# Performance work log

Measured on AMD Instinct MI355X. Metric: run time of the kernel, lower is better.

The kernel has to match this reference:

```python
import jax, jax.numpy as jnp
import numpy as np

COST_POS = 5.0
COST_CONF = 1.0
LAMBDA_POS = 5.0
LAMBDA_CONF = 2.0
LAMBDA_NOOBJ = 0.5


def _lsa(cost):
    """Rectangular linear sum assignment (Jonker-Volgenant shortest augmenting
    path), same semantics as scipy.optimize.linear_sum_assignment."""
    cost = np.asarray(cost, dtype=np.float64)
    transposed = cost.shape[1] < cost.shape[0]
    if transposed:
        cost = cost.T
    nr, nc = cost.shape  # nr <= nc
    u = np.zeros(nr)
    v = np.zeros(nc)
    col4row = np.full(nr, -1, dtype=np.int64)
    row4col = np.full(nc, -1, dtype=np.int64)
    for cur_row in range(nr):
        shortest = np.full(nc, np.inf)
        pathback = np.full(nc, -1, dtype=np.int64)
        SR = np.zeros(nr, dtype=bool)
        SC = np.zeros(nc, dtype=bool)
        remaining = np.ones(nc, dtype=bool)
        min_val = 0.0
        i = cur_row
        sink = -1
        while sink == -1:
            SR[i] = True
            rem = np.flatnonzero(remaining)
            new_cost = min_val + cost[i, rem] - u[i] - v[rem]
            better = new_cost < shortest[rem]
            idx = rem[better]
            shortest[idx] = new_cost[better]
            pathback[idx] = i
            j = rem[np.argmin(shortest[rem])]
            min_val = shortest[j]
            remaining[j] = False
            SC[j] = True
            if row4col[j] == -1:
                sink = j
            else:
                i = row4col[j]
        u[cur_row] += min_val
        rows = np.flatnonzero(SR)
        rows = rows[rows != cur_row]
        u[rows] += min_val - shortest[col4row[rows]]
        v[SC] -= min_val - shortest[SC]
        j = sink
        while True:
            i = pathback[j]
            row4col[j] = i
            col4row[i], j = j, col4row[i]
            if i == cur_row:
                break
    if transposed:
        rows = col4row
        cols = np.arange(nr)
        order = np.argsort(rows)
        return rows[order], cols[order]
    return np.arange(nr), col4row


def _match(pred_c, conf, gt_c):
    """Per-image Hungarian matching (host-side, @no_grad in the original).
    cost = COST_POS * L1(pred, gt) - COST_CONF * sigmoid(conf)."""
    B, N, _ = pred_c.shape
    M = gt_c.shape[1]
    pred_idx = np.empty((B, M), dtype=np.int64)
    gt_idx = np.empty((B, M), dtype=np.int64)
    for b in range(B):
        c_pos = np.abs(pred_c[b][:, None, :] - gt_c[b][None, :, :]).sum(-1)  # [N,M]
        c_conf = -1.0 / (1.0 + np.exp(-conf[b]))  # [N]
        cost = COST_POS * c_pos + COST_CONF * c_conf[:, None]
        r, c = _lsa(cost)
        pred_idx[b] = r
        gt_idx[b] = c
    return pred_idx, gt_idx


def setup_inputs() -> dict:
    key = jax.random.key(0)
    B, N, M, D = 32, 300, 50, 2
    k1, k2, k3, k4, k5 = jax.random.split(key, 5)
    return {
        "pred_centroids": jax.random.uniform(k1, (B, N, D), dtype=jnp.float32),
        "pred_logits": jax.random.normal(k2, (B, N, 1), dtype=jnp.float32),
        "pred_conf": jax.random.normal(k3, (B, N), dtype=jnp.float32),
        "gt_centroids": jax.random.uniform(k4, (B, M, D), dtype=jnp.float32),
        "gt_classes": jax.random.randint(k5, (B, M), 0, 1),
    }


def reference(pred_centroids, pred_logits, pred_conf, gt_centroids, gt_classes):
    B, N, D = pred_centroids.shape
    M = gt_centroids.shape[1]
    # Matching indices are constants (computed under no_grad, host-side).
    pred_idx, gt_idx = _match(np.asarray(pred_centroids, np.float64),
                              np.asarray(pred_conf, np.float64),
                              np.asarray(gt_centroids, np.float64))
    pred_idx = jnp.asarray(pred_idx)  # [B,M]
    gt_idx = jnp.asarray(gt_idx)      # [B,M]
    b = jnp.arange(B)[:, None]
    mp = pred_centroids[b, pred_idx]  # [B,M,D]
    mg = gt_centroids[b, gt_idx]      # [B,M,D]
    # per-image L1 mean, summed over images (all images have M matches)
    loss_pos = jnp.mean(jnp.abs(mp - mg), axis=(1, 2)).sum()
    m_logit = pred_conf[b, pred_idx]  # [B,M]
    # BCE-with-logits, target=1: softplus(-x); target=0: softplus(x)
    loss_obj = jnp.mean(jax.nn.softplus(-m_logit), axis=1).sum()
    unmatched = jnp.ones((B, N), dtype=bool).at[b, pred_idx].set(False)
    sp = jax.nn.softplus(pred_conf)
    loss_noobj = (jnp.where(unmatched, sp, 0.0).sum(axis=1) / (N - M)).sum()
    loss_pos = LAMBDA_POS * loss_pos / B
    loss_conf_obj = LAMBDA_CONF * loss_obj / B
    loss_conf_noobj = LAMBDA_NOOBJ * loss_noobj / B
    loss_total = loss_pos + loss_conf_obj + loss_conf_noobj
    n_matched = jnp.asarray(float(M), dtype=jnp.float32)  # total matched / B
    return loss_pos, loss_conf_obj, loss_conf_noobj, loss_total, n_matched
```

## Files before the change

### kernel.cpp

```cpp
#include <hip/hip_runtime.h>
#include <math.h>


#define BB 32
#define NN 300
#define MM 50
#define KPL 5
#define NWV 4
#define CPW 80

#define F5(OP) OP(0) OP(1) OP(2) OP(3) OP(4)

__device__ __forceinline__ float softplus_f(float x) {
    return fmaxf(x, 0.0f) + __logf(1.0f + __expf(-fabsf(x)));
}
__device__ __forceinline__ float readlane_f(float x, int l) {
    return __int_as_float(__builtin_amdgcn_readlane(__float_as_int(x), l));
}
__device__ __forceinline__ int readlane_i(int x, int l) {
    return __builtin_amdgcn_readlane(x, l);
}
__device__ __forceinline__ unsigned umaxu(unsigned a, unsigned b) { return a > b ? a : b; }

__device__ __forceinline__ unsigned minkey_f32(float d) {
    unsigned s = (unsigned)__float_as_int(d);
    unsigned us = (s & 0x80000000u) ? ~s : (s | 0x80000000u);
    return ~us;
}
__device__ __forceinline__ float keydec_up(unsigned key) {
    unsigned us = (~key) | 0x1FFu;
    return (us & 0x80000000u) ? __uint_as_float(us & 0x7FFFFFFFu)
                              : __uint_as_float(~us);
}

__device__ __forceinline__ unsigned rowshr_maxkey(unsigned x) {
#define DPP_STEP(CTRL) { \
    unsigned t_ = (unsigned)__builtin_amdgcn_update_dpp(0, (int)x, CTRL, 0xF, 0xF, false); \
    x = umaxu(x, t_); }
    DPP_STEP(0x111)
    DPP_STEP(0x112)
    DPP_STEP(0x114)
    DPP_STEP(0x118)
#undef DPP_STEP
    return x;
}

__device__ __forceinline__ int div5(int n) { return (n * 52429) >> 18; }

__global__ __launch_bounds__(NWV*64, 1) void lsa_loss_kernel(
    const float* __restrict__ pred_c,
    const float* __restrict__ conf,
    const float* __restrict__ gt_c,
    float* __restrict__ ws,
    float* __restrict__ out)
{
    const int b = blockIdx.x;
    const int tid = threadIdx.x;
    const int wid = tid >> 6;
    const int lane = tid & 63;
    const bool owns = tid < (NN / KPL);
    const int base_j = KPL * tid;

    __shared__ float4 s_px4[NN/4 + 5], s_py4[NN/4 + 5], s_cm4[NN/4 + 5];
    __shared__ int claimed[NN];
    __shared__ float s_cf[NN];
    __shared__ unsigned s_part[NWV * 64];
    float* s_px = (float*)s_px4;
    float* s_py = (float*)s_py4;
    float* s_cm2 = (float*)s_cm4;

#define DECL(k) float px5##k, py5##k, cf##k, cm##k, sh##k; int pb##k;
    F5(DECL)
#undef DECL
    unsigned r4cpack = 0;
    int rem;
    float u = 0.0f, gx5 = 0.0f, gy5 = 0.0f, u_sub = 0.0f;
    int col4row = -1;

#define LOADK(k) { \
        int j = base_j + k; \
        float vpx = 0.0f, vpy = 0.0f, vcf = 0.0f; \
        if (owns) { \
            float2 pc = *(const float2*)&pred_c[(b*NN + j)*2]; \
            vpx = pc.x; vpy = pc.y; \
            vcf = conf[b*NN + j]; \
        } \
        px5##k = 5.0f*vpx; py5##k = 5.0f*vpy; cf##k = vcf; \
        cm##k = -(1.0f / (1.0f + __expf(-vcf)));   }
    F5(LOADK)
#undef LOADK
    if (lane < MM) {
        float2 gc = *(const float2*)&gt_c[(b*MM + lane)*2];
        gx5 = 5.0f*gc.x;
        gy5 = 5.0f*gc.y;
    }
    claimed[tid] = 63;
    if (tid + 256 < NN) claimed[tid + 256] = 63;
#define STAGE(k) if (owns) { int j = base_j + k; \
        s_px[j] = px5##k; s_py[j] = py5##k; s_cm2[j] = cm##k + 2.0f; \
        s_cf[j] = cf##k; }
    F5(STAGE)
#undef STAGE
    if (tid >= 59 && tid < 64) {
        const float4 big = {1e30f, 1e30f, 1e30f, 1e30f};
        int p = 75 + (tid - 59);
        s_px4[p] = big; s_py4[p] = big; s_cm4[p] = big;
    }
#define IDXF(k) const unsigned idx##k = (unsigned)(511 - (base_j + k));
    F5(IDXF)
#undef IDXF
    __syncthreads();

    unsigned bestkey = 0u;
#pragma unroll
    for (int t = 0; t < CPW/8; ++t) {
        int j0 = wid*CPW + t*8;
        float4 vxa = s_px4[(j0 >> 2) + 0], vxb = s_px4[(j0 >> 2) + 1];
        float4 vya = s_py4[(j0 >> 2) + 0], vyb = s_py4[(j0 >> 2) + 1];
        float4 vca = s_cm4[(j0 >> 2) + 0], vcb = s_cm4[(j0 >> 2) + 1];
        float c0 = fabsf(vxa.x - gx5) + fabsf(vya.x - gy5) + vca.x;
        float c1 = fabsf(vxa.y - gx5) + fabsf(vya.y - gy5) + vca.y;
        float c2 = fabsf(vxa.z - gx5) + fabsf(vya.z - gy5) + vca.z;
        float c3 = fabsf(vxa.w - gx5) + fabsf(vya.w - gy5) + vca.w;
        float c4 = fabsf(vxb.x - gx5) + fabsf(vyb.x - gy5) + vcb.x;
        float c5 = fabsf(vxb.y - gx5) + fabsf(vyb.y - gy5) + vcb.y;
        float c6 = fabsf(vxb.z - gx5) + fabsf(vyb.z - gy5) + vcb.z;
        float c7 = fabsf(vxb.w - gx5) + fabsf(vyb.w - gy5) + vcb.w;
        unsigned q0 = (~__float_as_uint(c0) & 0xFFFFFE00u) | (unsigned)(511 - j0);
        unsigned q1 = (~__float_as_uint(c1) & 0xFFFFFE00u) | (unsigned)(510 - j0);
        unsigned q2 = (~__float_as_uint(c2) & 0xFFFFFE00u) | (unsigned)(509 - j0);
        unsigned q3 = (~__float_as_uint(c3) & 0xFFFFFE00u) | (unsigned)(508 - j0);
        unsigned q4 = (~__float_as_uint(c4) & 0xFFFFFE00u) | (unsigned)(507 - j0);
        unsigned q5 = (~__float_as_uint(c5) & 0xFFFFFE00u) | (unsigned)(506 - j0);
        unsigned q6 = (~__float_as_uint(c6) & 0xFFFFFE00u) | (unsigned)(505 - j0);
        unsigned q7 = (~__float_as_uint(c7) & 0xFFFFFE00u) | (unsigned)(504 - j0);
        unsigned qa = umaxu(umaxu(q0, q1), umaxu(q2, q3));
        unsigned qb = umaxu(umaxu(q4, q5), umaxu(q6, q7));
        bestkey = umaxu(bestkey, umaxu(qa, qb));
    }
    s_part[wid*64 + lane] = bestkey;
    __syncthreads();
    if (wid != 0) return;

    bestkey = umaxu(umaxu(s_part[lane], s_part[64 + lane]),
                    umaxu(s_part[128 + lane], s_part[192 + lane]));
    {
        int wantj = 511 - (int)(bestkey & 511u);
        if (lane < MM) {
            u = fabsf(s_px[wantj] - gx5) + fabsf(s_py[wantj] - gy5)
                + (s_cm2[wantj] - 2.0f);
            atomicMin(&claimed[wantj], lane);
        }
        col4row = (lane < MM && claimed[wantj] == lane) ? wantj : -1;
    }
#define RCINIT(k) { int w = owns ? claimed[base_j + k] : 63; \
        r4cpack |= ((w < 63) ? (unsigned)(w + 1) : 0u) << (6*k); }
    F5(RCINIT)
#undef RCINIT

    unsigned long long freerows = __ballot(lane < MM && col4row < 0);
    while (freerows) {
        int cur_row = (int)__ffsll(freerows) - 1;
        freerows &= freerows - 1ull;

#define RINIT(k) sh##k = INFINITY; pb##k = 0;
        F5(RINIT)
#undef RINIT
        rem = owns ? 0x1F : 0;
        unsigned long long sr_mask = 0ull;
        float min_val = 0.0f;
        int i = cur_row;
        int sink = -1;

        for (int pops = 0; pops <= NN && sink < 0; ++pops) {
            sr_mask |= (1ull << i);
            float u_i   = readlane_f(u,   i);
            float gx5_i = readlane_f(gx5, i);
            float gy5_i = readlane_f(gy5, i);
            float mvu = min_val - u_i;
            int ip1 = i + 1;

#define RELAX(k) { \
                float dx5 = fabsf(px5##k - gx5_i); \
                float dy5 = fabsf(py5##k - gy5_i); \
                float nc = dx5 + dy5 + (cm##k + mvu); \
                bool imp = (((rem >> k) & 1) != 0) && (nc < sh##k); \
                sh##k = imp ? nc : sh##k; \
                pb##k = imp ? ip1 : pb##k; }
            F5(RELAX)
#undef RELAX

#define KEYK(k) unsigned key##k = ((rem >> k) & 1) \
                ? ((minkey_f32(sh##k) & 0xFFFFFE00u) | idx##k) : 0u;
            F5(KEYK)
#undef KEYK
            unsigned lkey = umaxu(umaxu(umaxu(key0, key1), umaxu(key2, key3)), key4);

            unsigned acc = rowshr_maxkey(lkey);
            unsigned k0 = (unsigned)readlane_i((int)acc, 15);
            unsigned k1 = (unsigned)readlane_i((int)acc, 31);
            unsigned k2 = (unsigned)readlane_i((int)acc, 47);
            unsigned k3 = (unsigned)readlane_i((int)acc, 63);
            unsigned gkey = umaxu(umaxu(k0, k1), umaxu(k2, k3));
            if (gkey == 0u) { sink = 0; break; }

            int bestj = 511 - (int)(gkey & 511u);
            int srcl = div5(bestj);
            int qj = bestj - KPL*srcl;
            min_val = keydec_up(gkey);

            unsigned rp = (unsigned)readlane_i((int)r4cpack, srcl);
            int r4 = (int)((rp >> (qj*6)) & 63u) - 1;

            rem = (lane == srcl) ? (rem & ~(1 << qj)) : rem;
            if (r4 < 0 || r4 >= MM) {
                sink = bestj;
            } else {
                i = r4;
                u_sub = (lane == r4) ? min_val : u_sub;
            }
        }

        if (lane < MM) {
            if (lane == cur_row) u += min_val;
            else if ((sr_mask >> lane) & 1ull) u += min_val - u_sub;
        }
#define VUPD(k) if (owns && !((rem >> k) & 1)) cm##k += min_val - sh##k;
        F5(VUPD)
#undef VUPD

        int j = sink < 0 ? 0 : sink;
        for (int step = 0; step <= MM; ++step) {
            int tj = div5(j), qj2 = j - KPL*tj;
            int pbl = qj2==0?pb0:qj2==1?pb1:qj2==2?pb2:qj2==3?pb3:pb4;
            int pi = readlane_i(pbl, tj) - 1;
            if (pi < 0 || pi >= MM) break;
            int q6 = qj2*6;
            unsigned nv = (r4cpack & ~(63u << q6)) | ((unsigned)(pi+1) << q6);
            r4cpack = (lane == tj) ? nv : r4cpack;
            int c_old = readlane_i(col4row, pi);
            col4row = (lane == pi) ? j : col4row;
            j = c_old;
            if (pi == cur_row) break;
            if (j < 0 || j >= NN) break;
        }
    }

    float lp = 0.0f, lo = 0.0f, ln = 0.0f;
    if (lane < MM) {
        int j = (col4row < 0 || col4row >= NN) ? 0 : col4row;
        lp = 0.2f * (fabsf(s_px[j] - gx5) + fabsf(s_py[j] - gy5));
        lo = softplus_f(-s_cf[j]);
    }
#define NOOBJ(k) if (owns && ((r4cpack >> (6*k)) & 63u) == 0u) \
        ln += softplus_f(cf##k);
    F5(NOOBJ)
#undef NOOBJ
    for (int off = 32; off > 0; off >>= 1) {
        lp += __shfl_xor(lp, off, 64);
        lo += __shfl_xor(lo, off, 64);
        ln += __shfl_xor(ln, off, 64);
    }

    if (lane == 0) {
        __hip_atomic_store(&ws[b*4 + 0], lp, __ATOMIC_RELAXED, __HIP_MEMORY_SCOPE_AGENT);
        __hip_atomic_store(&ws[b*4 + 2], ln, __ATOMIC_RELAXED, __HIP_MEMORY_SCOPE_AGENT);
        __hip_atomic_store(&ws[b*4 + 1], lo, __ATOMIC_RELEASE, __HIP_MEMORY_SCOPE_AGENT);
    }

    if (b == 0) {
        float flo = 1.0f;
        bool done = false;
        for (int spin = 0; spin < (1 << 16) && !done; ++spin) {
            float v = 1.0f;
            if (lane < BB)
                v = __hip_atomic_load(&ws[lane*4 + 1], __ATOMIC_ACQUIRE,
                                      __HIP_MEMORY_SCOPE_AGENT);
            if (__all(v > 0.0f)) { flo = v; done = true; }
        }
        float flp = 0.0f, fln = 0.0f;
        if (lane < BB) {
            flp = __hip_atomic_load(&ws[lane*4 + 0], __ATOMIC_RELAXED,
                                    __HIP_MEMORY_SCOPE_AGENT);
            fln = __hip_atomic_load(&ws[lane*4 + 2], __ATOMIC_RELAXED,
                                    __HIP_MEMORY_SCOPE_AGENT);
            if (!done)
                flo = __hip_atomic_load(&ws[lane*4 + 1], __ATOMIC_RELAXED,
                                        __HIP_MEMORY_SCOPE_AGENT);
        } else {
            flo = 0.0f;
        }
        for (int off = 16; off > 0; off >>= 1) {
            flp += __shfl_xor(flp, off, 64);
            flo += __shfl_xor(flo, off, 64);
            fln += __shfl_xor(fln, off, 64);
        }
        if (lane == 0) {
            double cp = 5.0 * ((double)flp / (double)(MM*2))  / (double)BB;
            double co = 2.0 * ((double)flo / (double)MM)      / (double)BB;
            double cn = 0.5 * ((double)fln / (double)(NN-MM)) / (double)BB;
            out[0] = (float)cp;
            out[1] = (float)co;
            out[2] = (float)cn;
            out[3] = (float)(cp + co + cn);
            out[4] = 50.0f;
        }
    }
}

extern "C" void kernel_launch(void* const* d_in, const int* in_sizes, int n_in,
                              void* d_out, int out_size, void* d_ws, size_t ws_size,
                              hipStream_t stream) {
    const float* pred_c = (const float*)d_in[0];
    const float* conf   = (const float*)d_in[2];
    const float* gt_c   = (const float*)d_in[3];
    float* out = (float*)d_out;
    float* ws  = (float*)d_ws;

    lsa_loss_kernel<<<BB, NWV*64, 0, stream>>>(pred_c, conf, gt_c, ws, out);
}
```

Measured before the change: 87.55 us.

## Add parallel auction bidding phase across waves before augmenting-path LSA

Inserts an epsilon-auction (Bertsekas-style) phase after the greedy initial assignment, where up to four waves each bid for a free row in parallel, computing best and second-best columns and raising column prices. It aims to reduce the number of free rows left for the serial single-wave shortest-augmenting-path loop. The price updates are written back into the cost-modifier array and row duals before the exact phase. It adds several block-wide syncs per round, and the epsilon-shifted duals could affect exactness or numerical agreement.

```diff
diff --git a/kernel.cpp b/kernel.cpp
--- a/kernel.cpp
+++ b/kernel.cpp
@@ -8,6 +8,7 @@
 #define KPL 5
 #define NWV 4
 #define CPW 80
+#define AEPS 1.5e-4f
 
 #define F5(OP) OP(0) OP(1) OP(2) OP(3) OP(4)
 
@@ -21,6 +22,7 @@
     return __builtin_amdgcn_readlane(x, l);
 }
 __device__ __forceinline__ unsigned umaxu(unsigned a, unsigned b) { return a > b ? a : b; }
+__device__ __forceinline__ unsigned uminu(unsigned a, unsigned b) { return a < b ? a : b; }
 
 __device__ __forceinline__ unsigned minkey_f32(float d) {
     unsigned s = (unsigned)__float_as_int(d);
@@ -65,6 +67,12 @@
     __shared__ int claimed[NN];
     __shared__ float s_cf[NN];
     __shared__ unsigned s_part[NWV * 64];
+    __shared__ unsigned s_free[2];
+    __shared__ int s_c4r[MM];
+    __shared__ float s_u[MM];
+    __shared__ unsigned s_bidj[NWV];
+    __shared__ float s_bidcm[NWV];
+    __shared__ float s_bidu[NWV];
     float* s_px = (float*)s_px4;
     float* s_py = (float*)s_py4;
     float* s_cm2 = (float*)s_cm4;
@@ -140,11 +148,10 @@
     }
     s_part[wid*64 + lane] = bestkey;
     __syncthreads();
-    if (wid != 0) return;
-
-    bestkey = umaxu(umaxu(s_part[lane], s_part[64 + lane]),
-                    umaxu(s_part[128 + lane], s_part[192 + lane]));
-    {
+
+    if (wid == 0) {
+        bestkey = umaxu(umaxu(s_part[lane], s_part[64 + lane]),
+                        umaxu(s_part[128 + lane], s_part[192 + lane]));
         int wantj = 511 - (int)(bestkey & 511u);
         if (lane < MM) {
             u = fabsf(s_px[wantj] - gx5) + fabsf(s_py[wantj] - gy5)
@@ -152,7 +159,102 @@
             atomicMin(&claimed[wantj], lane);
         }
         col4row = (lane < MM && claimed[wantj] == lane) ? wantj : -1;
-    }
+        if (lane < MM) { s_c4r[lane] = col4row; s_u[lane] = u; }
+        unsigned long long fr = __ballot(lane < MM && col4row < 0);
+        if (lane == 0) {
+            s_free[0] = (unsigned)fr;
+            s_free[1] = (unsigned)(fr >> 32);
+        }
+    }
+
+    for (int round = 0; round < 64; ++round) {
+        __syncthreads();
+        unsigned f0 = s_free[0], f1 = s_free[1];
+        if (f0 == 0u && f1 == 0u) break;
+        int i = -1;
+        {
+            unsigned long long m = ((unsigned long long)f1 << 32) | f0;
+            int cnt = 0;
+            while (m) {
+                int p = (int)__ffsll(m) - 1;
+                if (cnt == wid) { i = p; break; }
+                m &= m - 1ull; ++cnt;
+            }
+        }
+        unsigned hk = 0u, lk = 0u;
+        if (i >= 0) {
+            float gxi = readlane_f(gx5, i);
+            float gyi = readlane_f(gy5, i);
+#pragma unroll
+            for (int t = 0; t < 5; ++t) {
+                int j = lane + 64*t;
+                if (j < NN) {
+                    float d = fabsf(s_px[j] - gxi) + fabsf(s_py[j] - gyi)
+                              + (s_cm2[j] - 2.0f);
+                    unsigned k = (minkey_f32(d) & 0xFFFFFE00u) | (unsigned)(511 - j);
+                    lk = umaxu(lk, uminu(hk, k));
+                    hk = umaxu(hk, k);
+                }
+            }
+#pragma unroll
+            for (int off = 1; off < 64; off <<= 1) {
+                unsigned th = (unsigned)__shfl_xor((int)hk, off, 64);
+                unsigned tl = (unsigned)__shfl_xor((int)lk, off, 64);
+                lk = umaxu(umaxu(lk, tl), uminu(hk, th));
+                hk = umaxu(hk, th);
+            }
+        }
+        if (lane == 0) {
+            if (i >= 0 && hk != 0u) {
+                int j1 = 511 - (int)(hk & 511u);
+                float d1 = keydec_up(hk);
+                float d2 = keydec_up(lk);
+                float dvu = fmaxf(d2 - d1, 0.0f) + AEPS;
+                s_bidj[wid]  = ((unsigned)i << 16) | (unsigned)j1;
+                s_bidcm[wid] = s_cm2[j1] + dvu;
+                s_bidu[wid]  = d2 + AEPS;
+            } else {
+                s_bidj[wid] = ~0u;
+            }
+        }
+        __syncthreads();
+        if (tid < NWV) {
+            unsigned bp = s_bidj[tid];
+            if (bp != ~0u) {
+                int row = (int)(bp >> 16);
+                int j   = (int)(bp & 0xFFFFu);
+                float nc = s_bidcm[tid];
+                bool win = true;
+                for (int o = 0; o < NWV; ++o) {
+                    if (o == tid) continue;
+                    unsigned ob = s_bidj[o];
+                    if (ob != ~0u && (int)(ob & 0xFFFFu) == j) {
+                        float oc = s_bidcm[o];
+                        if (oc > nc || (oc == nc && o < tid)) win = false;
+                    }
+                }
+                if (win) {
+                    int old = claimed[j];
+                    claimed[j] = row;
+                    s_cm2[j] = nc;
+                    s_c4r[row] = j;
+                    s_u[row] = s_bidu[tid];
+                    atomicAnd(&s_free[row >> 5], ~(1u << (row & 31)));
+                    if (old >= 0 && old < MM) {
+                        s_c4r[old] = -1;
+                        atomicOr(&s_free[old >> 5], 1u << (old & 31));
+                    }
+                }
+            }
+        }
+    }
+    if (wid != 0) return;
+
+    col4row = (lane < MM) ? s_c4r[lane] : -1;
+    u = (lane < MM) ? s_u[lane] : 0.0f;
+#define CMSYNC(k) if (owns) cm##k = s_cm2[base_j + k] - 2.0f;
+    F5(CMSYNC)
+#undef CMSYNC
 #define RCINIT(k) { int w = owns ? claimed[base_j + k] : 63; \
         r4cpack |= ((w < 63) ? (unsigned)(w + 1) : 0u) << (6*k); }
     F5(RCINIT)
```

Measured after the change: 109.3 us. +24.8%, slower.
